# Performance work log

Hardware: AMD Instinct MI355X
Metric: run time of the kernel (lower is better)

## Reference

```python
import jax, jax.numpy as jnp
import numpy as np

N_EMO = 524288   # number of rows (scaled-up emotion dim)
N_AU = 64        # total AU columns
N1 = 32          # size of loc1 (loc1 = [0:32], loc2 = [32:64])
ZERO_PAD = 1e-5  # conf.zeroPad
OCC_THRESH = 0.6


def setup_inputs() -> dict:
    key = jax.random.key(0)
    k1, k2, k3 = jax.random.split(key, 3)
    prob_all_au = jax.random.uniform(k1, (N_AU, 1), dtype=jnp.float32)
    EMO2AU_cpt = jax.random.uniform(k2, (N_EMO, N_AU), dtype=jnp.float32)
    # keep prob_AU away from 0 so prod(1/prob_AU) stays finite in fp32
    prob_AU_full = jax.random.uniform(k3, (N_AU, 1), dtype=jnp.float32,
                                      minval=0.3, maxval=0.9)
    return {"prob_all_au": prob_all_au, "EMO2AU_cpt": EMO2AU_cpt,
            "prob_AU_full": prob_AU_full}


def reference(prob_all_au, EMO2AU_cpt, prob_AU_full):
    # __init__: EMO2AU_cpt = where(cpt > 0, cpt, zeroPad), then column split
    E = jnp.where(EMO2AU_cpt > 0, EMO2AU_cpt, ZERO_PAD)
    E1, E2 = E[:, :N1], E[:, N1:]                      # dynamic / static parts
    negE1 = jnp.where(1.0 - E1 > 0, 1.0 - E1, ZERO_PAD)  # clamped in forward
    negE2 = 1.0 - E2                                      # registered unclamped

    p = prob_all_au[:, 0]
    p1, p2 = p[:N1], p[N1:]
    pA1, pA2 = prob_AU_full[:N1, 0], prob_AU_full[N1:, 0]

    # ---- dynamic (loc1) branch ----
    occ1 = (p1 > OCC_THRESH).astype(E.dtype)           # occ_mask1 (n1,)
    w_e1 = occ1 * E1 + (1.0 - occ1) * negE1            # (n_emo, n1)
    au1 = occ1 * p1 / pA1 + (1.0 - occ1) / pA1         # (n1,)
    weight1 = w_e1 * au1                               # (n_emo, n1)

    # ---- static (loc2) branch ----
    occ2 = (p2 > OCC_THRESH).astype(E.dtype)
    w_e2 = occ2 * E2 + (1.0 - occ2) * negE2
    au2 = occ2 / pA2 + (1.0 - occ2) / pA2              # == 1/pA2, kept faithful
    weight2 = w_e2 * au2

    # per-row product reduction (replaces the python loop + cat)
    prob_emo = jnp.prod(weight1, axis=1) * jnp.prod(weight2, axis=1)  # (n_emo,)
    out1 = prob_emo.reshape(1, -1)
    # F.normalize(p=1, dim=1) with eps=1e-12
    denom = jnp.maximum(jnp.sum(jnp.abs(out1), axis=1, keepdims=True), 1e-12)
    return out1 / denom
```

## Files before the change

kernel.cpp:

```cpp
#include <hip/hip_runtime.h>

constexpr int kNEmo = 524288;
constexpr int kNAu  = 64;
constexpr int kN1   = 32;


__global__ __launch_bounds__(64) void setup_consts(
    const float* __restrict__ prob_all_au,
    const float* __restrict__ prob_AU_full,
    float* __restrict__ cst)
{
    int j = threadIdx.x;
    float p   = prob_all_au[j];
    float pA  = prob_AU_full[j];
    bool  occ = p > 0.6f;
    float inv = 1.0f / pA;
    float s, c, f;
    if (j < kN1) {
        if (occ) { s = p / pA;  c = 0.0f; f = 0.0f; }
        else     { s = -inv;    c = inv;  f = inv * 1e-5f; }
    } else {
        if (occ) { s = inv;  c = 0.0f; }
        else     { s = -inv; c = inv;  }
        f = 0.0f;
    }
    cst[j]       = s;
    cst[64 + j]  = c;
    cst[128 + j] = f;
}

__global__ __launch_bounds__(256) void row_prod(
    const float* __restrict__ cpt,
    const float* __restrict__ cst,
    float* __restrict__ out,
    double* __restrict__ acc)
{
    __shared__ float s_s[64], s_c[64], s_f[64];
    int tid = threadIdx.x;
    if (tid < 64) {
        s_s[tid] = cst[tid];
        s_c[tid] = cst[64 + tid];
        s_f[tid] = cst[128 + tid];
    }
    __syncthreads();

    int row = blockIdx.x * 256 + tid;
    const float4* rp = reinterpret_cast<const float4*>(cpt) + (size_t)row * 16;

    float pr0 = 1.0f, pr1 = 1.0f, pr2 = 1.0f, pr3 = 1.0f;

#pragma unroll
    for (int k = 0; k < 16; ++k) {
        float4 v = rp[k];
        const int j = 4 * k;

        float E0 = (v.x > 0.0f) ? v.x : 1e-5f;
        float E1 = (v.y > 0.0f) ? v.y : 1e-5f;
        float E2 = (v.z > 0.0f) ? v.z : 1e-5f;
        float E3 = (v.w > 0.0f) ? v.w : 1e-5f;

        float w0 = fmaf(s_s[j + 0], E0, s_c[j + 0]);
        float w1 = fmaf(s_s[j + 1], E1, s_c[j + 1]);
        float w2 = fmaf(s_s[j + 2], E2, s_c[j + 2]);
        float w3 = fmaf(s_s[j + 3], E3, s_c[j + 3]);

        if (j < kN1) {
            w0 = fmaxf(w0, s_f[j + 0]);
            w1 = fmaxf(w1, s_f[j + 1]);
            w2 = fmaxf(w2, s_f[j + 2]);
            w3 = fmaxf(w3, s_f[j + 3]);
        }

        pr0 *= w0; pr1 *= w1; pr2 *= w2; pr3 *= w3;
    }

    float prod = (pr0 * pr1) * (pr2 * pr3);
    out[row] = prod;

    double val = fabs((double)prod);
#pragma unroll
    for (int off = 32; off > 0; off >>= 1)
        val += __shfl_down(val, off, 64);

    __shared__ double s_part[4];
    int wid = tid >> 6, lane = tid & 63;
    if (lane == 0) s_part[wid] = val;
    __syncthreads();
    if (tid == 0)
        atomicAdd(acc, s_part[0] + s_part[1] + s_part[2] + s_part[3]);
}

__global__ __launch_bounds__(256) void normalize(
    float* __restrict__ out, const double* __restrict__ acc)
{
    double s = *acc;
    if (!(s > 1e-12)) s = 1e-12;
    float invs = (float)(1.0 / s);

    int i = blockIdx.x * 256 + threadIdx.x;
    float4* o = reinterpret_cast<float4*>(out) + i;
    float4 v = *o;
    v.x *= invs; v.y *= invs; v.z *= invs; v.w *= invs;
    *o = v;
}

extern "C" void kernel_launch(void* const* d_in, const int* in_sizes, int n_in,
                              void* d_out, int out_size, void* d_ws, size_t ws_size,
                              hipStream_t stream)
{
    const float* prob_all_au  = (const float*)d_in[0];
    const float* cpt          = (const float*)d_in[1];
    const float* prob_AU_full = (const float*)d_in[2];
    float* out   = (float*)d_out;
    double* acc  = (double*)d_ws;
    float* cst   = (float*)((char*)d_ws + 256);

    hipMemsetAsync(d_ws, 0, 8, stream);

    setup_consts<<<1, 64, 0, stream>>>(prob_all_au, prob_AU_full, cst);
    row_prod<<<kNEmo / 256, 256, 0, stream>>>(cpt, cst, out, acc);
    normalize<<<kNEmo / 4 / 256, 256, 0, stream>>>(out, acc);
}
```

Baseline: 208.7 us.

## Coalesce row loads across lanes with butterfly shuffle product and fold constant setup

Each wavefront now reads its 64-row chunk with consecutive lanes loading consecutive float4s, replacing the per-thread strided row reads that were poorly coalesced. The per-row products are then rebuilt with a butterfly of xor shuffles, where lanes exchange partial products. The separate constant-setup kernel is removed: each lane computes its own four column constants in registers, which drops one launch and the shared-memory staging. The cost is extra shuffle work, some redundant constant arithmetic in every thread, and higher register pressure.

```diff
diff --git a/kernel.cpp b/kernel.cpp
--- a/kernel.cpp
+++ b/kernel.cpp
@@ -1,89 +1,89 @@
 #include <hip/hip_runtime.h>
+#include <float.h>
 
 constexpr int kNEmo = 524288;
-constexpr int kNAu  = 64;
-constexpr int kN1   = 32;
-
-
-__global__ __launch_bounds__(64) void setup_consts(
-    const float* __restrict__ prob_all_au,
-    const float* __restrict__ prob_AU_full,
-    float* __restrict__ cst)
-{
-    int j = threadIdx.x;
-    float p   = prob_all_au[j];
-    float pA  = prob_AU_full[j];
-    bool  occ = p > 0.6f;
-    float inv = 1.0f / pA;
-    float s, c, f;
-    if (j < kN1) {
-        if (occ) { s = p / pA;  c = 0.0f; f = 0.0f; }
-        else     { s = -inv;    c = inv;  f = inv * 1e-5f; }
-    } else {
-        if (occ) { s = inv;  c = 0.0f; }
-        else     { s = -inv; c = inv;  }
-        f = 0.0f;
-    }
-    cst[j]       = s;
-    cst[64 + j]  = c;
-    cst[128 + j] = f;
-}
 
 __global__ __launch_bounds__(256) void row_prod(
     const float* __restrict__ cpt,
-    const float* __restrict__ cst,
+    const float* __restrict__ prob_all_au,
+    const float* __restrict__ prob_AU_full,
     float* __restrict__ out,
     double* __restrict__ acc)
 {
-    __shared__ float s_s[64], s_c[64], s_f[64];
-    int tid = threadIdx.x;
-    if (tid < 64) {
-        s_s[tid] = cst[tid];
-        s_c[tid] = cst[64 + tid];
-        s_f[tid] = cst[128 + tid];
+    const int tid  = threadIdx.x;
+    const int lane = tid & 63;
+    const int wid  = tid >> 6;
+    const int q16  = lane & 15;
+
+    float cs[4], cc[4], cf[4];
+#pragma unroll
+    for (int q = 0; q < 4; ++q) {
+        int j = 4 * q16 + q;
+        float p   = prob_all_au[j];
+        float pA  = prob_AU_full[j];
+        float inv = 1.0f / pA;
+        bool  occ = p > 0.6f;
+        if (j < 32) {
+            if (occ) { cs[q] = p / pA; cc[q] = 0.0f; cf[q] = 0.0f; }
+            else     { cs[q] = -inv;   cc[q] = inv;  cf[q] = inv * 1e-5f; }
+        } else {
+            cs[q] = occ ?  inv : -inv;
+            cc[q] = occ ? 0.0f :  inv;
+            cf[q] = -FLT_MAX;
+        }
     }
-    __syncthreads();
 
-    int row = blockIdx.x * 256 + tid;
-    const float4* rp = reinterpret_cast<const float4*>(cpt) + (size_t)row * 16;
+    const int R = blockIdx.x * 256 + wid * 64;
+    const float4* base = reinterpret_cast<const float4*>(cpt) + (size_t)R * 16 + lane;
 
-    float pr0 = 1.0f, pr1 = 1.0f, pr2 = 1.0f, pr3 = 1.0f;
-
+    float part[16];
 #pragma unroll
-    for (int k = 0; k < 16; ++k) {
-        float4 v = rp[k];
-        const int j = 4 * k;
-
+    for (int i = 0; i < 16; ++i) {
+        float4 v = base[i * 64];
         float E0 = (v.x > 0.0f) ? v.x : 1e-5f;
         float E1 = (v.y > 0.0f) ? v.y : 1e-5f;
         float E2 = (v.z > 0.0f) ? v.z : 1e-5f;
         float E3 = (v.w > 0.0f) ? v.w : 1e-5f;
-
-        float w0 = fmaf(s_s[j + 0], E0, s_c[j + 0]);
-        float w1 = fmaf(s_s[j + 1], E1, s_c[j + 1]);
-        float w2 = fmaf(s_s[j + 2], E2, s_c[j + 2]);
-        float w3 = fmaf(s_s[j + 3], E3, s_c[j + 3]);
-
-        if (j < kN1) {
-            w0 = fmaxf(w0, s_f[j + 0]);
-            w1 = fmaxf(w1, s_f[j + 1]);
-            w2 = fmaxf(w2, s_f[j + 2]);
-            w3 = fmaxf(w3, s_f[j + 3]);
-        }
-
-        pr0 *= w0; pr1 *= w1; pr2 *= w2; pr3 *= w3;
+        float w0 = fmaxf(fmaf(cs[0], E0, cc[0]), cf[0]);
+        float w1 = fmaxf(fmaf(cs[1], E1, cc[1]), cf[1]);
+        float w2 = fmaxf(fmaf(cs[2], E2, cc[2]), cf[2]);
+        float w3 = fmaxf(fmaf(cs[3], E3, cc[3]), cf[3]);
+        part[i] = (w0 * w1) * (w2 * w3);
     }
 
-    float prod = (pr0 * pr1) * (pr2 * pr3);
-    out[row] = prod;
+    float s1[8];
+#pragma unroll
+    for (int i = 0; i < 8; ++i) {
+        float mine = (lane & 1) ? part[2*i]   : part[2*i+1];
+        float keep = (lane & 1) ? part[2*i+1] : part[2*i];
+        s1[i] = keep * __shfl_xor(mine, 1, 64);
+    }
+    float s2[4];
+#pragma unroll
+    for (int i = 0; i < 4; ++i) {
+        float mine = (lane & 2) ? s1[2*i]   : s1[2*i+1];
+        float keep = (lane & 2) ? s1[2*i+1] : s1[2*i];
+        s2[i] = keep * __shfl_xor(mine, 2, 64);
+    }
+    float s3[2];
+#pragma unroll
+    for (int i = 0; i < 2; ++i) {
+        float mine = (lane & 4) ? s2[2*i]   : s2[2*i+1];
+        float keep = (lane & 4) ? s2[2*i+1] : s2[2*i];
+        s3[i] = keep * __shfl_xor(mine, 4, 64);
+    }
+    float mine4 = (lane & 8) ? s3[0] : s3[1];
+    float keep4 = (lane & 8) ? s3[1] : s3[0];
+    float s4 = keep4 * __shfl_xor(mine4, 8, 64);
 
-    double val = fabs((double)prod);
+    out[R + 4 * (lane & 15) + (lane >> 4)] = s4;
+
+    double val = fabsf(s4);
 #pragma unroll
     for (int off = 32; off > 0; off >>= 1)
         val += __shfl_down(val, off, 64);
 
     __shared__ double s_part[4];
-    int wid = tid >> 6, lane = tid & 63;
     if (lane == 0) s_part[wid] = val;
     __syncthreads();
     if (tid == 0)
@@ -111,13 +111,11 @@
     const float* prob_all_au  = (const float*)d_in[0];
     const float* cpt          = (const float*)d_in[1];
     const float* prob_AU_full = (const float*)d_in[2];
-    float* out   = (float*)d_out;
-    double* acc  = (double*)d_ws;
-    float* cst   = (float*)((char*)d_ws + 256);
+    float*  out = (float*)d_out;
+    double* acc = (double*)d_ws;
 
     hipMemsetAsync(d_ws, 0, 8, stream);
 
-    setup_consts<<<1, 64, 0, stream>>>(prob_all_au, prob_AU_full, cst);
-    row_prod<<<kNEmo / 256, 256, 0, stream>>>(cpt, cst, out, acc);
+    row_prod<<<kNEmo / 256, 256, 0, stream>>>(cpt, prob_all_au, prob_AU_full, out, acc);
     normalize<<<kNEmo / 4 / 256, 256, 0, stream>>>(out, acc);
 }
```

After: 206.1 us. Within noise of the previous version (-1.3%).
